# Optimization experiments

Measured on AMD Instinct MI355X. Metric: run time of the kernel, lower is better.

Reference implementation:

```python
import jax, jax.numpy as jnp
import numpy as np


def fps(pts, m):
    # pts: [N,3]; iterative farthest point sampling, deterministic start at index 0
    d0 = jnp.sum((pts - pts[0]) ** 2, axis=-1)  # [N]
    def step(mind, _):
        nxt = jnp.argmax(mind)
        d = jnp.sum((pts - pts[nxt]) ** 2, axis=-1)
        return jnp.minimum(mind, d), nxt
    _, idxs = jax.lax.scan(step, d0, None, length=m - 1)
    return jnp.concatenate([jnp.zeros((1,), idxs.dtype), idxs])  # [m]


def knn(queries, pts, k):
    # queries [M,3], pts [N,3] -> [M,k] indices of k nearest points (includes self)
    d = (jnp.sum(queries ** 2, -1, keepdims=True)
         - 2.0 * queries @ pts.T
         + jnp.sum(pts ** 2, -1)[None, :])  # [M,N]
    _, idx = jax.lax.top_k(-d, k)
    return idx


def mlp(x, params):
    # shared PointNet MLP: Linear+ReLU stack
    for w, b in params:
        x = jax.nn.relu(x @ w + b)
    return x


def sa_level(points, feats, ratio, k, params):
    # set-abstraction: fps downsample -> knn group -> shared MLP -> max pool per cluster
    B, N, _ = points.shape
    m = int(N * ratio)
    sel = jax.vmap(lambda p: fps(p, m))(points)                      # [B,m]
    npts = jnp.take_along_axis(points, sel[..., None], axis=1)       # [B,m,3]
    nbr = jax.vmap(knn, in_axes=(0, 0, None))(npts, points, k)       # [B,m,k]
    C = feats.shape[-1]
    kf = jnp.take_along_axis(feats, nbr.reshape(B, m * k, 1), axis=1).reshape(B, m, k, C)
    h = mlp(kf, params)                                              # [B,m,k,out]
    return npts, jnp.max(h, axis=2)                                  # [B,m,3], [B,m,out]


def setup_inputs() -> dict:
    key = jax.random.key(0)
    ks = jax.random.split(key, 20)
    points = jax.random.normal(ks[0], (8, 8192, 3), dtype=jnp.float32)
    batch = jnp.repeat(jnp.arange(8, dtype=jnp.int64), 8192)
    dims = {
        'pn1': [(3, 8), (8, 16), (16, 16)],
        'pn2': [(16, 32), (32, 64), (64, 64)],
        'pn3': [(64, 128), (128, 256), (256, 256)],
    }
    inp = {'points': points, 'batch': batch}
    i = 1
    for name, shapes in dims.items():
        for j, (cin, cout) in enumerate(shapes, start=1):
            inp[f'{name}_w{j}'] = jax.random.normal(ks[i], (cin, cout), dtype=jnp.float32) * (1.0 / np.sqrt(cin))
            inp[f'{name}_b{j}'] = jnp.zeros((cout,), dtype=jnp.float32)
            i += 1
    return inp


def reference(points, batch,
              pn1_w1, pn1_b1, pn1_w2, pn1_b2, pn1_w3, pn1_b3,
              pn2_w1, pn2_b1, pn2_w2, pn2_b2, pn2_w3, pn2_b3,
              pn3_w1, pn3_b1, pn3_w2, pn3_b2, pn3_w3, pn3_b3):
    # batch is implied by the uniform [B,N,3] layout (all clouds equal size)
    p1 = [(pn1_w1, pn1_b1), (pn1_w2, pn1_b2), (pn1_w3, pn1_b3)]
    p2 = [(pn2_w1, pn2_b1), (pn2_w2, pn2_b2), (pn2_w3, pn2_b3)]
    p3 = [(pn3_w1, pn3_b1), (pn3_w2, pn3_b2), (pn3_w3, pn3_b3)]
    pts1, f1 = sa_level(points, points, 0.25, 4, p1)   # [8,2048,3], [8,2048,16]
    pts2, f2 = sa_level(pts1, f1, 0.25, 4, p2)         # [8,512,3], [8,512,64]
    # level 3: cluster == batch -> global max pool per cloud
    out = jnp.max(mlp(f2, p3), axis=1)                  # [8,256]
    return out
```

## Files before the change

### kernel.cpp

```cpp
#include <hip/hip_runtime.h>
#include <stdint.h>

typedef unsigned long long u64;
typedef unsigned int u32;
typedef float f2 __attribute__((ext_vector_type(2)));

__device__ __forceinline__ float rn_mul(float a, float b){ return __fmul_rn(a,b); }
__device__ __forceinline__ float rn_add(float a, float b){ return __fadd_rn(a,b); }
__device__ __forceinline__ float rn_sub(float a, float b){ return __fsub_rn(a,b); }

__device__ __forceinline__ u32 fkey(float d){
  u32 b = __float_as_uint(d);
  return b ^ ((u32)((int)b >> 31) | 0x80000000u);
}

__device__ __forceinline__ u64 shfl_xor64(u64 v, int mask){
  int lo = __shfl_xor((int)(u32)v, mask, 64);
  int hi = __shfl_xor((int)(u32)(v >> 32), mask, 64);
  return ((u64)(u32)hi << 32) | (u32)lo;
}
__device__ __forceinline__ u64 umin64(u64 a, u64 b){ return a < b ? a : b; }
__device__ __forceinline__ u64 umax64(u64 a, u64 b){ return a > b ? a : b; }

template<int C>
__device__ __forceinline__ u64 dstep64(u64 v){
  const u32 l = (u32)__builtin_amdgcn_update_dpp((int)(u32)v, (int)(u32)v, C, 0xF, 0xF, false);
  const u32 h = (u32)__builtin_amdgcn_update_dpp((int)(u32)(v>>32), (int)(u32)(v>>32), C, 0xF, 0xF, false);
  const u64 o = ((u64)h << 32) | l;
  return o > v ? o : v;
}
__device__ __forceinline__ u64 wave64_max64(u64 v){
  v = dstep64<0x111>(v);
  v = dstep64<0x112>(v);
  v = dstep64<0x114>(v);
  v = dstep64<0x118>(v);
  v = dstep64<0x142>(v);
  v = dstep64<0x143>(v);
  return v;
}
__device__ __forceinline__ u64 red8_max64(u64 v){
  v = dstep64<0x111>(v);
  v = dstep64<0x112>(v);
  v = dstep64<0x114>(v);
  const u32 l = (u32)__builtin_amdgcn_readlane((int)(u32)v, 7);
  const u32 h = (u32)__builtin_amdgcn_readlane((int)(u32)(v>>32), 7);
  return ((u64)h << 32) | l;
}

__device__ __forceinline__ f2 f2max(f2 a, f2 b){
  f2 r; r.x = fmaxf(a.x,b.x); r.y = fmaxf(a.y,b.y); return r;
}

template<int N, int NT, int M>
__global__ __launch_bounds__(NT)
void fps_kernel(const float* __restrict__ pts, float* __restrict__ npts)
{
#pragma clang fp contract(off)
  constexpr int PPT = N / NT;
  constexpr int PP2 = PPT / 2;
  constexpr int NW  = NT / 64;
  __shared__ float4 sp[N];
  __shared__ unsigned short WX[M];
  __shared__ u64 part[2][NW];
  const int b = blockIdx.x;
  const float* P = pts + (size_t)b * N * 3;
  float* O = npts + (size_t)b * M * 3;
  const int tid = threadIdx.x, lane = tid & 63, wv = tid >> 6;

  for (int i = tid; i < N; i += NT)
    sp[i] = make_float4(P[3*i+0], P[3*i+1], P[3*i+2], 0.0f);
  if (tid == 0) WX[0] = 0;
  __syncthreads();

  f2 rx[PP2], ry[PP2], rz[PP2], mind[PP2];
  const float4 c0 = sp[0];
  float bm;
  {
    const f2 cx2 = {c0.x,c0.x}, cy2 = {c0.y,c0.y}, cz2 = {c0.z,c0.z};
    f2 t[PP2];
#pragma unroll
    for (int j = 0; j < PP2; ++j){
      const float4 va = sp[tid + (2*j+0)*NT];
      const float4 vb = sp[tid + (2*j+1)*NT];
      rx[j] = f2{va.x, vb.x}; ry[j] = f2{va.y, vb.y}; rz[j] = f2{va.z, vb.z};
      const f2 dx = rx[j]-cx2, dy = ry[j]-cy2, dz = rz[j]-cz2;
      mind[j] = ((dx*dx) + (dy*dy)) + (dz*dz);
      t[j] = mind[j];
    }
#pragma unroll
    for (int s = PP2/2; s > 0; s >>= 1)
#pragma unroll
      for (int i = 0; i < s; ++i) t[i] = f2max(t[i], t[i+s]);
    bm = fmaxf(t[0].x, t[0].y);
  }

#define LANECAND(dst)                                                         \
  {                                                                           \
    u32 mo = 0xFFFFFFFFu;                                                     \
    _Pragma("unroll")                                                         \
    for (int j = PP2-1; j >= 0; --j){                                         \
      const u32 gb = (u32)(tid + (2*j+1)*NT);                                 \
      const u32 ga = (u32)(tid + (2*j+0)*NT);                                 \
      if (mind[j].y == bm) mo = gb;                                           \
      if (mind[j].x == bm) mo = ga;                                           \
    }                                                                         \
    (dst) = ((u64)__float_as_uint(bm) << 32) | (u64)(u32)~mo;                 \
  }

  u64 mypk;
  { u64 c; LANECAND(c); mypk = wave64_max64(c); }

  for (int it = 1; it < M; ++it){
    if (lane == 63) part[it & 1][wv] = mypk;
    __syncthreads();
    const u64 best = red8_max64(part[it & 1][lane & (NW-1)]);
    const u32 widx = ~(u32)best;
    if (tid == 0) WX[it] = (unsigned short)widx;
    const float4 c = sp[widx];
    const f2 cx2 = {c.x,c.x}, cy2 = {c.y,c.y}, cz2 = {c.z,c.z};
    f2 t[PP2];
#pragma unroll
    for (int j = 0; j < PP2; ++j){
      const f2 dx = rx[j]-cx2, dy = ry[j]-cy2, dz = rz[j]-cz2;
      const f2 d = ((dx*dx) + (dy*dy)) + (dz*dz);
      mind[j].x = fminf(mind[j].x, d.x);
      mind[j].y = fminf(mind[j].y, d.y);
      t[j] = mind[j];
    }
#pragma unroll
    for (int s = PP2/2; s > 0; s >>= 1)
#pragma unroll
      for (int i = 0; i < s; ++i) t[i] = f2max(t[i], t[i+s]);
    bm = fmaxf(t[0].x, t[0].y);
    u64 cand; LANECAND(cand);
    mypk = wave64_max64(cand);
  }
  __syncthreads();
  for (int j = tid; j < M; j += NT){
    const float4 v = sp[WX[j]];
    O[3*j+0] = v.x; O[3*j+1] = v.y; O[3*j+2] = v.z;
  }
#undef LANECAND
}

__device__ __forceinline__ void top4_insert(u64& a0,u64& a1,u64& a2,u64& a3, u64 p){
  if (p < a3){
    const bool c2 = p < a2, c1 = p < a1, c0 = p < a0;
    const u64 n3 = c2 ? a2 : p;
    const u64 n2 = c2 ? (c1 ? a1 : p) : a2;
    const u64 n1 = c1 ? (c0 ? a0 : p) : a1;
    const u64 n0 = c0 ? p : a0;
    a0=n0; a1=n1; a2=n2; a3=n3;
  }
}

__device__ __forceinline__ void merge4(u64& a0, u64& a1, u64& a2, u64& a3, int st)
{
  const u64 b0 = shfl_xor64(a0, st);
  const u64 b1 = shfl_xor64(a1, st);
  const u64 b2 = shfl_xor64(a2, st);
  const u64 b3 = shfl_xor64(a3, st);
  const u64 m0 = umin64(a0, b3);
  const u64 m1 = umin64(a1, b2);
  const u64 m2 = umin64(a2, b1);
  const u64 m3 = umin64(a3, b0);
  const u64 lo02 = umin64(m0,m2), hi02 = umax64(m0,m2);
  const u64 lo13 = umin64(m1,m3), hi13 = umax64(m1,m3);
  a0 = umin64(lo02, lo13); a1 = umax64(lo02, lo13);
  a2 = umin64(hi02, hi13); a3 = umax64(hi02, hi13);
}

template<int N, int M, int CH>
__global__ __launch_bounds__(256)
void knn_mlp1_kernel(const float* __restrict__ q, const float* __restrict__ pts,
                     const float* __restrict__ w1, const float* __restrict__ b1,
                     const float* __restrict__ w2, const float* __restrict__ b2,
                     const float* __restrict__ w3, const float* __restrict__ b3,
                     float* __restrict__ f1)
{
  __shared__ float4 s4[CH];
  constexpr int QPB = 64;
  const int blk = blockIdx.x;
  const int b = blk / (M / QPB);
  const int chunk = blk % (M / QPB);
  const int tid = threadIdx.x;
  const int g = tid >> 2;
  const int r = tid & 3;
  const int qi = chunk * QPB + g;
  const float* qp = q + ((size_t)b * M + qi) * 3;
  const float qx = qp[0], qy = qp[1], qz = qp[2];
  const float sumq = rn_add(rn_add(rn_mul(qx,qx), rn_mul(qy,qy)), rn_mul(qz,qz));
  const float* P = pts + (size_t)b * N * 3;

  u64 a0=~0ull, a1=~0ull, a2=~0ull, a3=~0ull;
  for (int c0 = 0; c0 < N; c0 += CH){
    for (int i = tid; i < CH; i += 256){
      const float x = P[3*(c0+i)+0], y = P[3*(c0+i)+1], z = P[3*(c0+i)+2];
      s4[i] = make_float4(x, y, z,
          rn_add(rn_add(rn_mul(x,x), rn_mul(y,y)), rn_mul(z,z)));
    }
    __syncthreads();
#pragma unroll 4
    for (int jj = r; jj < CH; jj += 4){
      const float4 v = s4[jj];
      const float dot = rn_add(rn_add(rn_mul(qx,v.x), rn_mul(qy,v.y)),
                               rn_mul(qz,v.z));
      const float d = rn_add(rn_sub(sumq, rn_mul(2.0f, dot)), v.w);
      top4_insert(a0,a1,a2,a3, ((u64)fkey(d) << 32) | (u32)(c0+jj));
    }
    __syncthreads();
  }
  merge4(a0,a1,a2,a3,1);
  merge4(a0,a1,a2,a3,2);
  const u64 selp = (r==0) ? a0 : (r==1) ? a1 : (r==2) ? a2 : a3;
  const u32 nidx = (u32)selp;

  const float nx = P[3*nidx+0], ny = P[3*nidx+1], nz = P[3*nidx+2];
  float h1[8];
#pragma unroll
  for (int c = 0; c < 8; ++c){
    float acc = b1[c];
    acc = fmaf(nx, w1[0*8+c], acc);
    acc = fmaf(ny, w1[1*8+c], acc);
    acc = fmaf(nz, w1[2*8+c], acc);
    h1[c] = fmaxf(acc, 0.0f);
  }
  float h2[16];
#pragma unroll
  for (int c = 0; c < 16; ++c){
    float acc = b2[c];
#pragma unroll
    for (int k = 0; k < 8; ++k) acc = fmaf(h1[k], w2[k*16+c], acc);
    h2[c] = fmaxf(acc, 0.0f);
  }
  float* fo = f1 + ((size_t)b * M + qi) * 16;
#pragma unroll
  for (int c = 0; c < 16; ++c){
    float acc = b3[c];
#pragma unroll
    for (int k = 0; k < 16; ++k) acc = fmaf(h2[k], w3[k*16+c], acc);
    float v = fmaxf(acc, 0.0f);
    v = fmaxf(v, __shfl_xor(v, 1, 64));
    v = fmaxf(v, __shfl_xor(v, 2, 64));
    if (r == 0) fo[c] = v;
  }
}

__global__ __launch_bounds__(256)
void knn_mlp2_kernel(const float* __restrict__ q, const float* __restrict__ pts,
                     const float* __restrict__ f1,
                     const float* __restrict__ w1, const float* __restrict__ b1,
                     const float* __restrict__ w2, const float* __restrict__ b2,
                     const float* __restrict__ w3, const float* __restrict__ b3,
                     float* __restrict__ f2)
{
  constexpr int N = 2048, M = 512, QPB = 64, QSTR = 2048;
  __shared__ float4 s4[N];
  const int blk = blockIdx.x;
  const int b = blk / (M / QPB);
  const int chunk = blk % (M / QPB);
  const int tid = threadIdx.x;
  const int g = tid >> 2;
  const int r = tid & 3;
  const int qi = chunk * QPB + g;
  const float* qp = q + ((size_t)b * QSTR + qi) * 3;
  const float qx = qp[0], qy = qp[1], qz = qp[2];
  const float sumq = rn_add(rn_add(rn_mul(qx,qx), rn_mul(qy,qy)), rn_mul(qz,qz));
  const float* P = pts + (size_t)b * N * 3;

  for (int i = tid; i < N; i += 256){
    const float x = P[3*i+0], y = P[3*i+1], z = P[3*i+2];
    s4[i] = make_float4(x, y, z,
        rn_add(rn_add(rn_mul(x,x), rn_mul(y,y)), rn_mul(z,z)));
  }
  __syncthreads();

  u64 a0=~0ull, a1=~0ull, a2=~0ull, a3=~0ull;
#pragma unroll 4
  for (int j = r; j < N; j += 4){
    const float4 v = s4[j];
    const float dot = rn_add(rn_add(rn_mul(qx,v.x), rn_mul(qy,v.y)),
                             rn_mul(qz,v.z));
    const float d = rn_add(rn_sub(sumq, rn_mul(2.0f, dot)), v.w);
    top4_insert(a0,a1,a2,a3, ((u64)fkey(d) << 32) | (u32)j);
  }
  merge4(a0,a1,a2,a3,1);
  merge4(a0,a1,a2,a3,2);
  const u64 selp = (r==0) ? a0 : (r==1) ? a1 : (r==2) ? a2 : a3;
  const u32 nidx = (u32)selp;

  const float* fv = f1 + ((size_t)b * 2048 + nidx) * 16;
  float x[16];
#pragma unroll
  for (int i = 0; i < 4; ++i){
    const float4 v = ((const float4*)fv)[i];
    x[4*i+0]=v.x; x[4*i+1]=v.y; x[4*i+2]=v.z; x[4*i+3]=v.w;
  }
  float h1[32];
#pragma unroll
  for (int c = 0; c < 32; ++c){
    float acc = b1[c];
#pragma unroll
    for (int k = 0; k < 16; ++k) acc = fmaf(x[k], w1[k*32+c], acc);
    h1[c] = fmaxf(acc, 0.0f);
  }
  float h2[64];
#pragma unroll
  for (int c = 0; c < 64; ++c){
    float acc = b2[c];
#pragma unroll
    for (int k = 0; k < 32; ++k) acc = fmaf(h1[k], w2[k*64+c], acc);
    h2[c] = fmaxf(acc, 0.0f);
  }
  float* fo = f2 + ((size_t)b * M + qi) * 64;
#pragma unroll
  for (int c = 0; c < 64; ++c){
    float acc = b3[c];
#pragma unroll
    for (int k = 0; k < 64; ++k) acc = fmaf(h2[k], w3[k*64+c], acc);
    float v = fmaxf(acc, 0.0f);
    v = fmaxf(v, __shfl_xor(v, 1, 64));
    v = fmaxf(v, __shfl_xor(v, 2, 64));
    if (r == 0) fo[c] = v;
  }
}

__global__ __launch_bounds__(256)
void mlp3_kernel(const float* __restrict__ f2,
                 const float* __restrict__ w1, const float* __restrict__ b1,
                 const float* __restrict__ w2, const float* __restrict__ b2,
                 const float* __restrict__ w3, const float* __restrict__ b3,
                 float* __restrict__ out)
{
  constexpr int P = 16;
  __shared__ float X [P][64];
  __shared__ float H1[P][128];
  __shared__ float H2[P][256];
  __shared__ float PM[4][256];
  const int blk = blockIdx.x;
  const int b  = blk >> 5;
  const int pc = blk & 31;
  const int tid = threadIdx.x;
  const float* F = f2 + ((size_t)b * 512 + (size_t)pc * P) * 64;
  { const float4 v = ((const float4*)F)[tid]; ((float4*)&X[0][0])[tid] = v; }
  __syncthreads();
  {
    const int p = tid >> 4, c0 = (tid & 15) * 8;
    float acc[8];
#pragma unroll
    for (int i = 0; i < 8; ++i) acc[i] = b1[c0+i];
    for (int k = 0; k < 64; ++k){
      const float xv = X[p][k];
      const float4 wa = *(const float4*)&w1[k*128 + c0];
      const float4 wb = *(const float4*)&w1[k*128 + c0 + 4];
      acc[0]=fmaf(xv,wa.x,acc[0]); acc[1]=fmaf(xv,wa.y,acc[1]);
      acc[2]=fmaf(xv,wa.z,acc[2]); acc[3]=fmaf(xv,wa.w,acc[3]);
      acc[4]=fmaf(xv,wb.x,acc[4]); acc[5]=fmaf(xv,wb.y,acc[5]);
      acc[6]=fmaf(xv,wb.z,acc[6]); acc[7]=fmaf(xv,wb.w,acc[7]);
    }
#pragma unroll
    for (int i = 0; i < 8; ++i) H1[p][c0+i] = fmaxf(acc[i], 0.0f);
  }
  __syncthreads();
  {
    const int p = tid >> 4, c0 = (tid & 15) * 16;
    float acc[16];
#pragma unroll
    for (int i = 0; i < 16; ++i) acc[i] = b2[c0+i];
    for (int k = 0; k < 128; ++k){
      const float xv = H1[p][k];
#pragma unroll
      for (int i4 = 0; i4 < 4; ++i4){
        const float4 wv = *(const float4*)&w2[k*256 + c0 + 4*i4];
        acc[4*i4+0]=fmaf(xv,wv.x,acc[4*i4+0]);
        acc[4*i4+1]=fmaf(xv,wv.y,acc[4*i4+1]);
        acc[4*i4+2]=fmaf(xv,wv.z,acc[4*i4+2]);
        acc[4*i4+3]=fmaf(xv,wv.w,acc[4*i4+3]);
      }
    }
#pragma unroll
    for (int i = 0; i < 16; ++i) H2[p][c0+i] = fmaxf(acc[i], 0.0f);
  }
  __syncthreads();
  {
    const int pg = tid >> 6, c0 = (tid & 63) * 4;
    float acc[4][4];
#pragma unroll
    for (int p4 = 0; p4 < 4; ++p4)
#pragma unroll
      for (int i = 0; i < 4; ++i) acc[p4][i] = b3[c0+i];
    for (int k = 0; k < 256; ++k){
      const float4 wv = *(const float4*)&w3[k*256 + c0];
#pragma unroll
      for (int p4 = 0; p4 < 4; ++p4){
        const float xv = H2[pg*4+p4][k];
        acc[p4][0]=fmaf(xv,wv.x,acc[p4][0]);
        acc[p4][1]=fmaf(xv,wv.y,acc[p4][1]);
        acc[p4][2]=fmaf(xv,wv.z,acc[p4][2]);
        acc[p4][3]=fmaf(xv,wv.w,acc[p4][3]);
      }
    }
    float4 mx;
    mx.x = fmaxf(fmaxf(fmaxf(acc[0][0],0.f),fmaxf(acc[1][0],0.f)),
                 fmaxf(fmaxf(acc[2][0],0.f),fmaxf(acc[3][0],0.f)));
    mx.y = fmaxf(fmaxf(fmaxf(acc[0][1],0.f),fmaxf(acc[1][1],0.f)),
                 fmaxf(fmaxf(acc[2][1],0.f),fmaxf(acc[3][1],0.f)));
    mx.z = fmaxf(fmaxf(fmaxf(acc[0][2],0.f),fmaxf(acc[1][2],0.f)),
                 fmaxf(fmaxf(acc[2][2],0.f),fmaxf(acc[3][2],0.f)));
    mx.w = fmaxf(fmaxf(fmaxf(acc[0][3],0.f),fmaxf(acc[1][3],0.f)),
                 fmaxf(fmaxf(acc[2][3],0.f),fmaxf(acc[3][3],0.f)));
    *(float4*)&PM[pg][c0] = mx;
  }
  __syncthreads();
  {
    const float m = fmaxf(fmaxf(PM[0][tid], PM[1][tid]),
                          fmaxf(PM[2][tid], PM[3][tid]));
    atomicMax((int*)(out + b*256 + tid), __float_as_int(m));
  }
}

extern "C" void kernel_launch(void* const* d_in, const int* in_sizes, int n_in,
                              void* d_out, int out_size, void* d_ws, size_t ws_size,
                              hipStream_t stream)
{
  const float* pts  = (const float*)d_in[0];
  const float* p1w1 = (const float*)d_in[2];
  const float* p1b1 = (const float*)d_in[3];
  const float* p1w2 = (const float*)d_in[4];
  const float* p1b2 = (const float*)d_in[5];
  const float* p1w3 = (const float*)d_in[6];
  const float* p1b3 = (const float*)d_in[7];
  const float* p2w1 = (const float*)d_in[8];
  const float* p2b1 = (const float*)d_in[9];
  const float* p2w2 = (const float*)d_in[10];
  const float* p2b2 = (const float*)d_in[11];
  const float* p2w3 = (const float*)d_in[12];
  const float* p2b3 = (const float*)d_in[13];
  const float* p3w1 = (const float*)d_in[14];
  const float* p3b1 = (const float*)d_in[15];
  const float* p3w2 = (const float*)d_in[16];
  const float* p3b2 = (const float*)d_in[17];
  const float* p3w3 = (const float*)d_in[18];
  const float* p3b3 = (const float*)d_in[19];

  float* ws = (float*)d_ws;
  size_t o = 0;
  float* npts1 = ws + o; o += (size_t)8*2048*3;
  float* f1    = ws + o; o += (size_t)8*2048*16;
  float* f2    = ws + o; o += (size_t)8*512*64;

  fps_kernel<8192,512,2048><<<8, 512, 0, stream>>>(pts, npts1);
  knn_mlp1_kernel<8192,2048,2048><<<8*32, 256, 0, stream>>>(npts1, pts,
      p1w1, p1b1, p1w2, p1b2, p1w3, p1b3, f1);
  knn_mlp2_kernel<<<8*8, 256, 0, stream>>>(npts1, npts1, f1,
      p2w1, p2b1, p2w2, p2b2, p2w3, p2b3, f2);
  hipMemsetAsync(d_out, 0, (size_t)out_size * sizeof(float), stream);
  mlp3_kernel<<<8*32, 256, 0, stream>>>(f2,
      p3w1, p3b1, p3w2, p3b2, p3w3, p3b3, (float*)d_out);
}
```

Measured before the change: 2.252 ms.

## Shrink FPS block, pack argmax as u64 tree, dual top-4 lists in kNN

The FPS kernel now runs with 256 threads, so each thread holds more points in registers. The cross-wave reduction shrinks to 4 waves using two DPP steps and a readlane. The per-lane argmax becomes a u64 max tree over (distance, inverted index) packs instead of a float max followed by equality scans. Both kNN kernels keep two independent top-4 lists over interleaved points and merge them at the end, which shortens the dependent insert chain. The cost is higher register pressure: the FPS kernel needs 2x the per-thread point registers plus a PPT-wide u64 array, which may cause spills, and the block has fewer threads hiding latency on a serial loop.

```diff
diff --git a/kernel.cpp b/kernel.cpp
--- a/kernel.cpp
+++ b/kernel.cpp
@@ -30,25 +30,9 @@
   return o > v ? o : v;
 }
 __device__ __forceinline__ u64 wave64_max64(u64 v){
-  v = dstep64<0x111>(v);
-  v = dstep64<0x112>(v);
-  v = dstep64<0x114>(v);
-  v = dstep64<0x118>(v);
-  v = dstep64<0x142>(v);
-  v = dstep64<0x143>(v);
+  v = dstep64<0x111>(v); v = dstep64<0x112>(v); v = dstep64<0x114>(v);
+  v = dstep64<0x118>(v); v = dstep64<0x142>(v); v = dstep64<0x143>(v);
   return v;
-}
-__device__ __forceinline__ u64 red8_max64(u64 v){
-  v = dstep64<0x111>(v);
-  v = dstep64<0x112>(v);
-  v = dstep64<0x114>(v);
-  const u32 l = (u32)__builtin_amdgcn_readlane((int)(u32)v, 7);
-  const u32 h = (u32)__builtin_amdgcn_readlane((int)(u32)(v>>32), 7);
-  return ((u64)h << 32) | l;
-}
-
-__device__ __forceinline__ f2 f2max(f2 a, f2 b){
-  f2 r; r.x = fmaxf(a.x,b.x); r.y = fmaxf(a.y,b.y); return r;
 }
 
 template<int N, int NT, int M>
@@ -74,10 +58,8 @@
 
   f2 rx[PP2], ry[PP2], rz[PP2], mind[PP2];
   const float4 c0 = sp[0];
-  float bm;
   {
     const f2 cx2 = {c0.x,c0.x}, cy2 = {c0.y,c0.y}, cz2 = {c0.z,c0.z};
-    f2 t[PP2];
 #pragma unroll
     for (int j = 0; j < PP2; ++j){
       const float4 va = sp[tid + (2*j+0)*NT];
@@ -85,62 +67,51 @@
       rx[j] = f2{va.x, vb.x}; ry[j] = f2{va.y, vb.y}; rz[j] = f2{va.z, vb.z};
       const f2 dx = rx[j]-cx2, dy = ry[j]-cy2, dz = rz[j]-cz2;
       mind[j] = ((dx*dx) + (dy*dy)) + (dz*dz);
-      t[j] = mind[j];
-    }
-#pragma unroll
-    for (int s = PP2/2; s > 0; s >>= 1)
-#pragma unroll
-      for (int i = 0; i < s; ++i) t[i] = f2max(t[i], t[i+s]);
-    bm = fmaxf(t[0].x, t[0].y);
-  }
-
-#define LANECAND(dst)                                                         \
+    }
+  }
+
+#define LANEPK(dstpk)                                                         \
   {                                                                           \
-    u32 mo = 0xFFFFFFFFu;                                                     \
+    u64 p_[PPT];                                                              \
     _Pragma("unroll")                                                         \
-    for (int j = PP2-1; j >= 0; --j){                                         \
-      const u32 gb = (u32)(tid + (2*j+1)*NT);                                 \
-      const u32 ga = (u32)(tid + (2*j+0)*NT);                                 \
-      if (mind[j].y == bm) mo = gb;                                           \
-      if (mind[j].x == bm) mo = ga;                                           \
+    for (int k = 0; k < PPT; ++k){                                            \
+      const float mk = (k&1) ? mind[k>>1].y : mind[k>>1].x;                   \
+      p_[k] = ((u64)__float_as_uint(mk) << 32)                                \
+            | (u64)(u32)~(u32)(tid + k*NT);                                   \
     }                                                                         \
-    (dst) = ((u64)__float_as_uint(bm) << 32) | (u64)(u32)~mo;                 \
-  }
-
-  u64 mypk;
-  { u64 c; LANECAND(c); mypk = wave64_max64(c); }
+    _Pragma("unroll")                                                         \
+    for (int s = PPT/2; s > 0; s >>= 1)                                       \
+      for (int i = 0; i < s; ++i) p_[i] = umax64(p_[i], p_[i+s]);             \
+    (dstpk) = wave64_max64(p_[0]);                                            \
+  }
+
+  u64 mypk; LANEPK(mypk)
 
   for (int it = 1; it < M; ++it){
     if (lane == 63) part[it & 1][wv] = mypk;
     __syncthreads();
-    const u64 best = red8_max64(part[it & 1][lane & (NW-1)]);
-    const u32 widx = ~(u32)best;
+    u64 v = part[it & 1][lane & (NW-1)];
+    v = dstep64<0x111>(v); v = dstep64<0x112>(v);
+    const u32 wl = (u32)__builtin_amdgcn_readlane((int)(u32)v, 3);
+    const u32 widx = ~wl;
     if (tid == 0) WX[it] = (unsigned short)widx;
     const float4 c = sp[widx];
     const f2 cx2 = {c.x,c.x}, cy2 = {c.y,c.y}, cz2 = {c.z,c.z};
-    f2 t[PP2];
 #pragma unroll
     for (int j = 0; j < PP2; ++j){
       const f2 dx = rx[j]-cx2, dy = ry[j]-cy2, dz = rz[j]-cz2;
       const f2 d = ((dx*dx) + (dy*dy)) + (dz*dz);
       mind[j].x = fminf(mind[j].x, d.x);
       mind[j].y = fminf(mind[j].y, d.y);
-      t[j] = mind[j];
-    }
-#pragma unroll
-    for (int s = PP2/2; s > 0; s >>= 1)
-#pragma unroll
-      for (int i = 0; i < s; ++i) t[i] = f2max(t[i], t[i+s]);
-    bm = fmaxf(t[0].x, t[0].y);
-    u64 cand; LANECAND(cand);
-    mypk = wave64_max64(cand);
+    }
+    LANEPK(mypk)
   }
   __syncthreads();
   for (int j = tid; j < M; j += NT){
     const float4 v = sp[WX[j]];
     O[3*j+0] = v.x; O[3*j+1] = v.y; O[3*j+2] = v.z;
   }
-#undef LANECAND
+#undef LANEPK
 }
 
 __device__ __forceinline__ void top4_insert(u64& a0,u64& a1,u64& a2,u64& a3, u64 p){
@@ -154,12 +125,8 @@
   }
 }
 
-__device__ __forceinline__ void merge4(u64& a0, u64& a1, u64& a2, u64& a3, int st)
-{
-  const u64 b0 = shfl_xor64(a0, st);
-  const u64 b1 = shfl_xor64(a1, st);
-  const u64 b2 = shfl_xor64(a2, st);
-  const u64 b3 = shfl_xor64(a3, st);
+__device__ __forceinline__ void merge4_local(u64& a0,u64& a1,u64& a2,u64& a3,
+                                             u64 b0,u64 b1,u64 b2,u64 b3){
   const u64 m0 = umin64(a0, b3);
   const u64 m1 = umin64(a1, b2);
   const u64 m2 = umin64(a2, b1);
@@ -168,6 +135,15 @@
   const u64 lo13 = umin64(m1,m3), hi13 = umax64(m1,m3);
   a0 = umin64(lo02, lo13); a1 = umax64(lo02, lo13);
   a2 = umin64(hi02, hi13); a3 = umax64(hi02, hi13);
+}
+
+__device__ __forceinline__ void merge4(u64& a0, u64& a1, u64& a2, u64& a3, int st)
+{
+  const u64 b0 = shfl_xor64(a0, st);
+  const u64 b1 = shfl_xor64(a1, st);
+  const u64 b2 = shfl_xor64(a2, st);
+  const u64 b3 = shfl_xor64(a3, st);
+  merge4_local(a0,a1,a2,a3, b0,b1,b2,b3);
 }
 
 template<int N, int M, int CH>
@@ -193,6 +169,7 @@
   const float* P = pts + (size_t)b * N * 3;
 
   u64 a0=~0ull, a1=~0ull, a2=~0ull, a3=~0ull;
+  u64 e0=~0ull, e1=~0ull, e2=~0ull, e3=~0ull;
   for (int c0 = 0; c0 < N; c0 += CH){
     for (int i = tid; i < CH; i += 256){
       const float x = P[3*(c0+i)+0], y = P[3*(c0+i)+1], z = P[3*(c0+i)+2];
@@ -200,16 +177,22 @@
           rn_add(rn_add(rn_mul(x,x), rn_mul(y,y)), rn_mul(z,z)));
     }
     __syncthreads();
-#pragma unroll 4
-    for (int jj = r; jj < CH; jj += 4){
-      const float4 v = s4[jj];
-      const float dot = rn_add(rn_add(rn_mul(qx,v.x), rn_mul(qy,v.y)),
-                               rn_mul(qz,v.z));
-      const float d = rn_add(rn_sub(sumq, rn_mul(2.0f, dot)), v.w);
-      top4_insert(a0,a1,a2,a3, ((u64)fkey(d) << 32) | (u32)(c0+jj));
+#pragma unroll 2
+    for (int jj = r; jj < CH; jj += 8){
+      { const float4 v = s4[jj];
+        const float dot = rn_add(rn_add(rn_mul(qx,v.x), rn_mul(qy,v.y)),
+                                 rn_mul(qz,v.z));
+        const float d = rn_add(rn_sub(sumq, rn_mul(2.0f, dot)), v.w);
+        top4_insert(a0,a1,a2,a3, ((u64)fkey(d) << 32) | (u32)(c0+jj)); }
+      { const float4 v = s4[jj+4];
+        const float dot = rn_add(rn_add(rn_mul(qx,v.x), rn_mul(qy,v.y)),
+                                 rn_mul(qz,v.z));
+        const float d = rn_add(rn_sub(sumq, rn_mul(2.0f, dot)), v.w);
+        top4_insert(e0,e1,e2,e3, ((u64)fkey(d) << 32) | (u32)(c0+jj+4)); }
     }
     __syncthreads();
   }
+  merge4_local(a0,a1,a2,a3, e0,e1,e2,e3);
   merge4(a0,a1,a2,a3,1);
   merge4(a0,a1,a2,a3,2);
   const u64 selp = (r==0) ? a0 : (r==1) ? a1 : (r==2) ? a2 : a3;
@@ -276,14 +259,21 @@
   __syncthreads();
 
   u64 a0=~0ull, a1=~0ull, a2=~0ull, a3=~0ull;
-#pragma unroll 4
-  for (int j = r; j < N; j += 4){
-    const float4 v = s4[j];
-    const float dot = rn_add(rn_add(rn_mul(qx,v.x), rn_mul(qy,v.y)),
-                             rn_mul(qz,v.z));
-    const float d = rn_add(rn_sub(sumq, rn_mul(2.0f, dot)), v.w);
-    top4_insert(a0,a1,a2,a3, ((u64)fkey(d) << 32) | (u32)j);
-  }
+  u64 e0=~0ull, e1=~0ull, e2=~0ull, e3=~0ull;
+#pragma unroll 2
+  for (int j = r; j < N; j += 8){
+    { const float4 v = s4[j];
+      const float dot = rn_add(rn_add(rn_mul(qx,v.x), rn_mul(qy,v.y)),
+                               rn_mul(qz,v.z));
+      const float d = rn_add(rn_sub(sumq, rn_mul(2.0f, dot)), v.w);
+      top4_insert(a0,a1,a2,a3, ((u64)fkey(d) << 32) | (u32)j); }
+    { const float4 v = s4[j+4];
+      const float dot = rn_add(rn_add(rn_mul(qx,v.x), rn_mul(qy,v.y)),
+                               rn_mul(qz,v.z));
+      const float d = rn_add(rn_sub(sumq, rn_mul(2.0f, dot)), v.w);
+      top4_insert(e0,e1,e2,e3, ((u64)fkey(d) << 32) | (u32)(j+4)); }
+  }
+  merge4_local(a0,a1,a2,a3, e0,e1,e2,e3);
   merge4(a0,a1,a2,a3,1);
   merge4(a0,a1,a2,a3,2);
   const u64 selp = (r==0) ? a0 : (r==1) ? a1 : (r==2) ? a2 : a3;
@@ -449,7 +439,7 @@
   float* f1    = ws + o; o += (size_t)8*2048*16;
   float* f2    = ws + o; o += (size_t)8*512*64;
 
-  fps_kernel<8192,512,2048><<<8, 512, 0, stream>>>(pts, npts1);
+  fps_kernel<8192,256,2048><<<8, 256, 0, stream>>>(pts, npts1);
   knn_mlp1_kernel<8192,2048,2048><<<8*32, 256, 0, stream>>>(npts1, pts,
       p1w1, p1b1, p1w2, p1b2, p1w3, p1b3, f1);
   knn_mlp2_kernel<<<8*8, 256, 0, stream>>>(npts1, npts1, f1,
```

After: 2.268 ms. About the same (+0.7%).
